# Kernel tuning notes

Measured on AMD Instinct MI355X. Metric: run time of the kernel, lower is better.

Reference implementation:

```python
import jax, jax.numpy as jnp
import numpy as np

N_HEADS = 16
WINDOW = 128
EPS = 1e-6
NEG_INF = -1e30  # effectively -inf after softmax in fp32


def setup_inputs() -> dict:
    key = jax.random.key(0)
    ks = jax.random.split(key, 5)
    B, T, D = 2, 2048, 1024
    scale = 1.0 / np.sqrt(D)
    return {
        "x": jax.random.normal(ks[0], (B, T, D), dtype=jnp.float32),
        "Wq": jax.random.normal(ks[1], (D, D), dtype=jnp.float32) * scale,
        "Wk": jax.random.normal(ks[2], (D, D), dtype=jnp.float32) * scale,
        "Wv": jax.random.normal(ks[3], (D, D), dtype=jnp.float32) * scale,
        "Wo": jax.random.normal(ks[4], (D, D), dtype=jnp.float32) * scale,
    }


def _l2norm(t):
    # torch F.normalize: t / max(||t||, eps)
    n = jnp.sqrt(jnp.sum(t * t, axis=-1, keepdims=True))
    return t / jnp.maximum(n, EPS)


def reference(x, Wq, Wk, Wv, Wo):
    B, T, D = x.shape
    H, hd = N_HEADS, D // N_HEADS
    # projections (torch Linear: x @ W.T), split heads -> [B, H, T, hd]
    def proj(W):
        return jnp.einsum('btd,ed->bte', x, W).reshape(B, T, H, hd).transpose(0, 2, 1, 3)
    q = _l2norm(proj(Wq))
    k = _l2norm(proj(Wk))
    v = proj(Wv)
    # scores [B, H, T, T] (no 1/sqrt(d) scale in the source)
    attn = jnp.einsum('bhqd,bhkd->bhqk', q, k)
    pos = jnp.arange(T)
    rel = pos[None, :] - pos[:, None]            # rel[i, j] = j - i
    mask = (rel < 0) | (rel >= WINDOW)           # allowed: 0 <= j-i < window
    base = jnp.linspace(0.0, 1.0, H, dtype=x.dtype)
    slopes = jnp.power(jnp.asarray(2.0, x.dtype), -(8.0 * base))  # [H]
    alibi = -jnp.abs(rel).astype(x.dtype)[None, :, :] * slopes[:, None, None]  # [H,T,T]
    bias = jnp.where(mask[None, :, :], jnp.asarray(NEG_INF, x.dtype), alibi)
    attn = jax.nn.softmax(attn + bias[None], axis=-1)
    out = jnp.einsum('bhqk,bhkd->bhqd', attn, v)
    out = out.transpose(0, 2, 1, 3).reshape(B, T, D)
    return jnp.einsum('btd,ed->bte', out, Wo)
```

## Files before the change

### kernel.cpp

```cpp
#include <hip/hip_runtime.h>
#include <hip/hip_bf16.h>

#define T_SEQ   2048
#define BATCH   2
#define DMODEL  1024
#define NHEADS  16
#define HDIM    64
#define WINDOW  128

typedef __attribute__((ext_vector_type(8))) short bf16x8;
typedef __attribute__((ext_vector_type(4))) float f32x4;

__device__ inline void unpack8(uint4 u, float* f) {
    unsigned int w[4] = {u.x, u.y, u.z, u.w};
#pragma unroll
    for (int i = 0; i < 4; i++) {
        f[2*i]   = __uint_as_float(w[i] << 16);
        f[2*i+1] = __uint_as_float(w[i] & 0xffff0000u);
    }
}

__device__ inline void gld_lds16(const __hip_bfloat16* g, __hip_bfloat16* l) {
    __builtin_amdgcn_global_load_lds(
        (const __attribute__((address_space(1))) unsigned int*)g,
        (__attribute__((address_space(3))) unsigned int*)l, 16, 0, 0);
}

__global__ __launch_bounds__(256) void cvt_kernel(
    const float* __restrict__ x,  const float* __restrict__ Wq,
    const float* __restrict__ Wk, const float* __restrict__ Wv,
    const float* __restrict__ Wo,
    __hip_bfloat16* __restrict__ xb, __hip_bfloat16* __restrict__ Wb)
{
    const int slot = blockIdx.y;
    const float* src;
    __hip_bfloat16* dst;
    int n;
    if (slot == 0) { src = x; dst = xb; n = 4 * 1024 * 1024; }
    else {
        src = (slot == 1) ? Wq : (slot == 2) ? Wk : (slot == 3) ? Wv : Wo;
        dst = Wb + (size_t)(slot - 1) * 1024 * 1024;
        n = 1024 * 1024;
    }
    int i = (blockIdx.x * 256 + threadIdx.x) * 8;
    if (i >= n) return;
    float4 a = *(const float4*)(src + i);
    float4 b = *(const float4*)(src + i + 4);
    __hip_bfloat16 pk[8] = {
        __float2bfloat16(a.x), __float2bfloat16(a.y),
        __float2bfloat16(a.z), __float2bfloat16(a.w),
        __float2bfloat16(b.x), __float2bfloat16(b.y),
        __float2bfloat16(b.z), __float2bfloat16(b.w)};
    *(uint4*)(dst + i) = *(uint4*)pk;
}

__global__ __launch_bounds__(256) void gemm_qkv(
    const __hip_bfloat16* __restrict__ A,
    const __hip_bfloat16* __restrict__ W0,
    const __hip_bfloat16* __restrict__ W1,
    const __hip_bfloat16* __restrict__ W2,
    __hip_bfloat16* __restrict__ C0,
    __hip_bfloat16* __restrict__ C1,
    __hip_bfloat16* __restrict__ C2,
    int M, int N, int K)
{
    const int z = blockIdx.z;
    const __hip_bfloat16* W = (z == 0) ? W0 : (z == 1 ? W1 : W2);
    __hip_bfloat16* C = (z == 0) ? C0 : (z == 1 ? C1 : C2);

    const int n0 = blockIdx.x * 128;
    const int m0 = blockIdx.y * 128;

    __shared__ __hip_bfloat16 As[128 * 32];
    __shared__ __hip_bfloat16 Bs[128 * 32];

    const int t    = threadIdx.x;
    const int lane = t & 63;
    const int wv   = t >> 6;

    const int gc   = ((lane & 3) - (lane >> 3)) & 3;
    const int srow = wv * 32 + (lane >> 2);
    const __hip_bfloat16* Ag = A + (size_t)(m0 + srow) * K + gc * 8;
    const __hip_bfloat16* Wg = W + (size_t)(n0 + srow) * K + gc * 8;
    const size_t row16 = (size_t)16 * K;
    __hip_bfloat16* AsD0 = &As[(wv * 32) * 32];
    __hip_bfloat16* AsD1 = &As[(wv * 32 + 16) * 32];
    __hip_bfloat16* BsD0 = &Bs[(wv * 32) * 32];
    __hip_bfloat16* BsD1 = &Bs[(wv * 32 + 16) * 32];

    const int wm   = (wv >> 1) * 64;
    const int wn   = (wv & 1) * 64;
    const int lrow = lane & 15;
    const int quad = lane >> 4;
    const int slot = ((quad + (lrow >> 1)) & 3) * 8;

    f32x4 acc[4][4];
#pragma unroll
    for (int i = 0; i < 4; i++)
#pragma unroll
        for (int j = 0; j < 4; j++)
            acc[i][j] = (f32x4){0.f, 0.f, 0.f, 0.f};

    for (int k0 = 0; k0 < K; k0 += 32) {
        gld_lds16(Ag + k0,         AsD0);
        gld_lds16(Ag + k0 + row16, AsD1);
        gld_lds16(Wg + k0,         BsD0);
        gld_lds16(Wg + k0 + row16, BsD1);
        __syncthreads();

        bf16x8 af[4], bfv[4];
#pragma unroll
        for (int mi = 0; mi < 4; mi++)
            af[mi] = *(const bf16x8*)&As[(wm + mi * 16 + lrow) * 32 + slot];
#pragma unroll
        for (int ni = 0; ni < 4; ni++)
            bfv[ni] = *(const bf16x8*)&Bs[(wn + ni * 16 + lrow) * 32 + slot];
#pragma unroll
        for (int mi = 0; mi < 4; mi++)
#pragma unroll
            for (int ni = 0; ni < 4; ni++)
                acc[mi][ni] = __builtin_amdgcn_mfma_f32_16x16x32_bf16(
                    af[mi], bfv[ni], acc[mi][ni], 0, 0, 0);
        __syncthreads();
    }

    if (z != 2) {
#pragma unroll
        for (int mi = 0; mi < 4; mi++) {
#pragma unroll
            for (int rr = 0; rr < 4; rr++) {
                float ss = 0.f;
#pragma unroll
                for (int ni = 0; ni < 4; ni++)
                    ss += acc[mi][ni][rr] * acc[mi][ni][rr];
                ss += __shfl_xor(ss, 1);
                ss += __shfl_xor(ss, 2);
                ss += __shfl_xor(ss, 4);
                ss += __shfl_xor(ss, 8);
                float inv = 1.0f / fmaxf(sqrtf(ss), 1e-6f);
#pragma unroll
                for (int ni = 0; ni < 4; ni++)
                    acc[mi][ni][rr] *= inv;
            }
        }
    }

#pragma unroll
    for (int mi = 0; mi < 4; mi++) {
#pragma unroll
        for (int rr = 0; rr < 4; rr++) {
            int row = m0 + wm + mi * 16 + quad * 4 + rr;
            __hip_bfloat16* Crow = C + (size_t)row * N + n0 + wn + lrow;
#pragma unroll
            for (int ni = 0; ni < 4; ni++)
                Crow[ni * 16] = __float2bfloat16(acc[mi][ni][rr]);
        }
    }
}

__global__ __launch_bounds__(256) void gemm_o(
    const __hip_bfloat16* __restrict__ A,
    const __hip_bfloat16* __restrict__ W,
    float* __restrict__ C,
    int M, int N, int K)
{
    const int n0 = blockIdx.x * 128;
    const int m0 = blockIdx.y * 64;

    __shared__ __hip_bfloat16 As[64 * 32];
    __shared__ __hip_bfloat16 Bs[128 * 32];

    const int t    = threadIdx.x;
    const int lane = t & 63;
    const int wv   = t >> 6;

    const int gc    = ((lane & 3) - (lane >> 3)) & 3;
    const int srowA = wv * 16 + (lane >> 2);
    const int srowB = wv * 32 + (lane >> 2);
    const __hip_bfloat16* Ag = A + (size_t)(m0 + srowA) * K + gc * 8;
    const __hip_bfloat16* Wg = W + (size_t)(n0 + srowB) * K + gc * 8;
    const size_t row16 = (size_t)16 * K;
    __hip_bfloat16* AsD0 = &As[(wv * 16) * 32];
    __hip_bfloat16* BsD0 = &Bs[(wv * 32) * 32];
    __hip_bfloat16* BsD1 = &Bs[(wv * 32 + 16) * 32];

    const int wm   = (wv >> 1) * 32;
    const int wn   = (wv & 1) * 64;
    const int lrow = lane & 15;
    const int quad = lane >> 4;
    const int slot = ((quad + (lrow >> 1)) & 3) * 8;

    f32x4 acc[2][4];
#pragma unroll
    for (int i = 0; i < 2; i++)
#pragma unroll
        for (int j = 0; j < 4; j++)
            acc[i][j] = (f32x4){0.f, 0.f, 0.f, 0.f};

    for (int k0 = 0; k0 < K; k0 += 32) {
        gld_lds16(Ag + k0, AsD0);
        gld_lds16(Wg + k0,         BsD0);
        gld_lds16(Wg + k0 + row16, BsD1);
        __syncthreads();

        bf16x8 af[2], bfv[4];
#pragma unroll
        for (int mi = 0; mi < 2; mi++)
            af[mi] = *(const bf16x8*)&As[(wm + mi * 16 + lrow) * 32 + slot];
#pragma unroll
        for (int ni = 0; ni < 4; ni++)
            bfv[ni] = *(const bf16x8*)&Bs[(wn + ni * 16 + lrow) * 32 + slot];
#pragma unroll
        for (int mi = 0; mi < 2; mi++)
#pragma unroll
            for (int ni = 0; ni < 4; ni++)
                acc[mi][ni] = __builtin_amdgcn_mfma_f32_16x16x32_bf16(
                    af[mi], bfv[ni], acc[mi][ni], 0, 0, 0);
        __syncthreads();
    }

#pragma unroll
    for (int mi = 0; mi < 2; mi++) {
#pragma unroll
        for (int rr = 0; rr < 4; rr++) {
            int row = m0 + wm + mi * 16 + quad * 4 + rr;
            float* Crow = C + (size_t)row * N + n0 + wn + lrow;
#pragma unroll
            for (int ni = 0; ni < 4; ni++)
                Crow[ni * 16] = acc[mi][ni][rr];
        }
    }
}

__global__ __launch_bounds__(256) void attn_kernel(
    const __hip_bfloat16* __restrict__ Q,
    const __hip_bfloat16* __restrict__ K,
    const __hip_bfloat16* __restrict__ V,
    __hip_bfloat16* __restrict__ O)
{
    const int i0 = blockIdx.x * 64;
    const int h  = blockIdx.y;
    const int b  = blockIdx.z;

    __shared__ __hip_bfloat16 Ks[192 * 72];
    __shared__ __hip_bfloat16 Vt[64 * 200];

    const size_t base = ((size_t)b * T_SEQ) * DMODEL + h * HDIM;
    const int t = threadIdx.x;

    for (int task = t; task < 192 * 8; task += 256) {
        int row = task >> 3;
        int c   = task & 7;
        int j   = min(i0 + row, T_SEQ - 1);
        *(uint4*)&Ks[row * 72 + c * 8] = *(const uint4*)(K + base + (size_t)j * DMODEL + c * 8);
    }
    for (int task = t; task < 192; task += 256) {
        int c  = task & 7;
        int r0 = (task >> 3) * 8;
        int b0 = task >> 3;
        unsigned short m[8][8];
#pragma unroll
        for (int i = 0; i < 8; i++) {
            int j = min(i0 + r0 + i, T_SEQ - 1);
            uint4 u = *(const uint4*)(V + base + (size_t)j * DMODEL + c * 8);
            unsigned short tmp[8];
            *(uint4*)tmp = u;
#pragma unroll
            for (int e = 0; e < 8; e++) m[e][i] = tmp[e];
        }
#pragma unroll
        for (int e = 0; e < 8; e++) {
            int d  = c * 8 + e;
            int sg = (b0 & ~7) | ((b0 + (d >> 3)) & 7);
            *(uint4*)&Vt[d * 200 + sg * 8] = *(uint4*)m[e];
        }
    }
    for (int task = t; task < 64; task += 256) {
        uint4 zz = {0, 0, 0, 0};
        *(uint4*)&Vt[task * 200 + 192] = zz;
    }
    __syncthreads();

    const int lane = t & 63;
    const int w    = t >> 6;
    const int col  = lane & 15;
    const int quad = lane >> 4;
    const float slope = exp2f(-8.0f * (float)h / 15.0f);

    const __hip_bfloat16* qp = Q + base + (size_t)(i0 + w * 16 + col) * DMODEL + quad * 8;
    bf16x8 qf0 = *(const bf16x8*)(qp);
    bf16x8 qf1 = *(const bf16x8*)(qp + 32);

    f32x4 sc[9];
#pragma unroll
    for (int kt = 0; kt < 9; kt++) {
        sc[kt] = (f32x4){0.f, 0.f, 0.f, 0.f};
        const __hip_bfloat16* kr = &Ks[(w * 16 + kt * 16 + col) * 72 + quad * 8];
        bf16x8 kb0 = *(const bf16x8*)(kr);
        bf16x8 kb1 = *(const bf16x8*)(kr + 32);
        sc[kt] = __builtin_amdgcn_mfma_f32_16x16x32_bf16(qf0, kb0, sc[kt], 0, 0, 0);
        sc[kt] = __builtin_amdgcn_mfma_f32_16x16x32_bf16(qf1, kb1, sc[kt], 0, 0, 0);
    }

    float mx[4] = {-3e38f, -3e38f, -3e38f, -3e38f};
#pragma unroll
    for (int kt = 0; kt < 9; kt++) {
#pragma unroll
        for (int r = 0; r < 4; r++) {
            int ql  = quad * 4 + r;
            int rel = kt * 16 + col - ql;
            int ka  = i0 + w * 16 + kt * 16 + col;
            bool valid = (rel >= 0) && (rel < WINDOW) && (ka < T_SEQ);
            float v = valid ? (sc[kt][r] - (float)rel * slope) : -1e30f;
            sc[kt][r] = v;
            mx[r] = fmaxf(mx[r], v);
        }
    }
#pragma unroll
    for (int r = 0; r < 4; r++) {
        mx[r] = fmaxf(mx[r], __shfl_xor(mx[r], 1));
        mx[r] = fmaxf(mx[r], __shfl_xor(mx[r], 2));
        mx[r] = fmaxf(mx[r], __shfl_xor(mx[r], 4));
        mx[r] = fmaxf(mx[r], __shfl_xor(mx[r], 8));
    }
    float sm[4] = {0.f, 0.f, 0.f, 0.f};
#pragma unroll
    for (int kt = 0; kt < 9; kt++) {
#pragma unroll
        for (int r = 0; r < 4; r++) {
            float e = __expf(sc[kt][r] - mx[r]);
            sc[kt][r] = e;
            sm[r] += e;
        }
    }
#pragma unroll
    for (int r = 0; r < 4; r++) {
        sm[r] += __shfl_xor(sm[r], 1);
        sm[r] += __shfl_xor(sm[r], 2);
        sm[r] += __shfl_xor(sm[r], 4);
        sm[r] += __shfl_xor(sm[r], 8);
        sm[r] = 1.0f / sm[r];
    }

    __syncthreads();
    __hip_bfloat16* Ps = Ks + w * (16 * 168);
#pragma unroll
    for (int kt = 0; kt < 9; kt++)
#pragma unroll
        for (int r = 0; r < 4; r++)
            Ps[(quad * 4 + r) * 168 + kt * 16 + col] = __float2bfloat16(sc[kt][r] * sm[r]);
#pragma unroll
    for (int i = 0; i < 4; i++)
        Ps[(lane & 15) * 168 + 144 + quad * 4 + i] = __float2bfloat16(0.f);
    __syncthreads();

    f32x4 o[4];
#pragma unroll
    for (int nd = 0; nd < 4; nd++) o[nd] = (f32x4){0.f, 0.f, 0.f, 0.f};
#pragma unroll
    for (int kc = 0; kc < 5; kc++) {
        bf16x8 pf = *(const bf16x8*)&Ps[col * 168 + kc * 32 + quad * 8];
        int bblk = w * 2 + kc * 4 + quad;
#pragma unroll
        for (int nd = 0; nd < 4; nd++) {
            int d  = nd * 16 + col;
            int sg = (bblk < 24) ? ((bblk & ~7) | ((bblk + (d >> 3)) & 7)) : 24;
            bf16x8 vf = *(const bf16x8*)&Vt[d * 200 + sg * 8];
            o[nd] = __builtin_amdgcn_mfma_f32_16x16x32_bf16(pf, vf, o[nd], 0, 0, 0);
        }
    }

#pragma unroll
    for (int r = 0; r < 4; r++) {
        __hip_bfloat16* op = O + base + (size_t)(i0 + w * 16 + quad * 4 + r) * DMODEL + col;
#pragma unroll
        for (int nd = 0; nd < 4; nd++)
            op[nd * 16] = __float2bfloat16(o[nd][r]);
    }
}

extern "C" void kernel_launch(void* const* d_in, const int* in_sizes, int n_in,
                              void* d_out, int out_size, void* d_ws, size_t ws_size,
                              hipStream_t stream)
{
    const float* x  = (const float*)d_in[0];
    const float* Wq = (const float*)d_in[1];
    const float* Wk = (const float*)d_in[2];
    const float* Wv = (const float*)d_in[3];
    const float* Wo = (const float*)d_in[4];
    float* out = (float*)d_out;

    const size_t MT = (size_t)BATCH * T_SEQ;
    __hip_bfloat16* Qw = (__hip_bfloat16*)d_ws;
    __hip_bfloat16* Kw = Qw + MT * DMODEL;
    __hip_bfloat16* Vw = Kw + MT * DMODEL;
    __hip_bfloat16* XA = Vw + MT * DMODEL;
    __hip_bfloat16* Wb = XA + MT * DMODEL;

    cvt_kernel<<<dim3(2048, 5), 256, 0, stream>>>(x, Wq, Wk, Wv, Wo, XA, Wb);

    dim3 g1(DMODEL / 128, MT / 128, 3);
    gemm_qkv<<<g1, 256, 0, stream>>>(
        XA, Wb, Wb + 1024 * 1024, Wb + 2 * 1024 * 1024,
        Qw, Kw, Vw, (int)MT, DMODEL, DMODEL);

    dim3 g2(T_SEQ / 64, NHEADS, BATCH);
    attn_kernel<<<g2, 256, 0, stream>>>(Qw, Kw, Vw, XA);

    dim3 g3(DMODEL / 128, MT / 64, 1);
    gemm_o<<<g3, 256, 0, stream>>>(
        XA, Wb + 3 * 1024 * 1024, out, (int)MT, DMODEL, DMODEL);
}
```

Before: 155.7 us.

## Remap GEMM tiles per XCD and load attention K via direct-to-LDS swizzle

Both GEMMs now derive tile coordinates from a linearized block id so that consecutive blocks dispatched to the same XCD cover a compact M×N region. This is meant to improve L2 reuse of A and W rows within each XCD's cache. The attention kernel loads its K tile with global_load_lds into an unpadded, XOR-style swizzled LDS layout instead of staging through registers into a padded layout. The MFMA reads use the matching swizzle. This cuts register traffic and LDS footprint, but the new mappings assume specific grid dimensions.

```diff
diff --git a/kernel.cpp b/kernel.cpp
--- a/kernel.cpp
+++ b/kernel.cpp
@@ -64,12 +64,19 @@
     __hip_bfloat16* __restrict__ C2,
     int M, int N, int K)
 {
-    const int z = blockIdx.z;
+    const int lid   = blockIdx.x + 8 * blockIdx.y + 256 * blockIdx.z;
+    const int xcd   = lid & 7;
+    const int s     = lid >> 3;
+    const int m_loc = s & 7;
+    const int rest  = s >> 3;
+    const int n_loc = rest & 3;
+    const int z     = rest >> 2;
+
     const __hip_bfloat16* W = (z == 0) ? W0 : (z == 1 ? W1 : W2);
     __hip_bfloat16* C = (z == 0) ? C0 : (z == 1 ? C1 : C2);
 
-    const int n0 = blockIdx.x * 128;
-    const int m0 = blockIdx.y * 128;
+    const int m0 = ((xcd & 3) * 8 + m_loc) * 128;
+    const int n0 = ((xcd >> 2) * 4 + n_loc) * 128;
 
     __shared__ __hip_bfloat16 As[128 * 32];
     __shared__ __hip_bfloat16 Bs[128 * 32];
@@ -164,8 +171,14 @@
     float* __restrict__ C,
     int M, int N, int K)
 {
-    const int n0 = blockIdx.x * 128;
-    const int m0 = blockIdx.y * 64;
+    const int lid   = blockIdx.x + 8 * blockIdx.y;
+    const int xcd   = lid & 7;
+    const int s     = lid >> 3;
+    const int m_loc = s & 15;
+    const int n_loc = s >> 4;
+
+    const int m0 = ((xcd & 3) * 16 + m_loc) * 64;
+    const int n0 = ((xcd >> 2) * 4 + n_loc) * 128;
 
     __shared__ __hip_bfloat16 As[64 * 32];
     __shared__ __hip_bfloat16 Bs[128 * 32];
@@ -242,17 +255,24 @@
     const int h  = blockIdx.y;
     const int b  = blockIdx.z;
 
-    __shared__ __hip_bfloat16 Ks[192 * 72];
+    __shared__ __hip_bfloat16 Ks[192 * 64];
     __shared__ __hip_bfloat16 Vt[64 * 200];
 
     const size_t base = ((size_t)b * T_SEQ) * DMODEL + h * HDIM;
-    const int t = threadIdx.x;
-
-    for (int task = t; task < 192 * 8; task += 256) {
-        int row = task >> 3;
-        int c   = task & 7;
-        int j   = min(i0 + row, T_SEQ - 1);
-        *(uint4*)&Ks[row * 72 + c * 8] = *(const uint4*)(K + base + (size_t)j * DMODEL + c * 8);
+    const int t    = threadIdx.x;
+    const int lane = t & 63;
+    const int w    = t >> 6;
+
+    {
+        const int drow = lane >> 3, sl = lane & 7;
+#pragma unroll
+        for (int inst = 0; inst < 6; inst++) {
+            int r0 = w * 48 + inst * 8;
+            int r  = r0 + drow;
+            int gcx = (sl - r) & 7;
+            int j  = min(i0 + r, T_SEQ - 1);
+            gld_lds16(K + base + (size_t)j * DMODEL + gcx * 8, &Ks[r0 * 64]);
+        }
     }
     for (int task = t; task < 192; task += 256) {
         int c  = task & 7;
@@ -281,8 +301,6 @@
     }
     __syncthreads();
 
-    const int lane = t & 63;
-    const int w    = t >> 6;
     const int col  = lane & 15;
     const int quad = lane >> 4;
     const float slope = exp2f(-8.0f * (float)h / 15.0f);
@@ -295,9 +313,9 @@
 #pragma unroll
     for (int kt = 0; kt < 9; kt++) {
         sc[kt] = (f32x4){0.f, 0.f, 0.f, 0.f};
-        const __hip_bfloat16* kr = &Ks[(w * 16 + kt * 16 + col) * 72 + quad * 8];
-        bf16x8 kb0 = *(const bf16x8*)(kr);
-        bf16x8 kb1 = *(const bf16x8*)(kr + 32);
+        int r = w * 16 + kt * 16 + col;
+        bf16x8 kb0 = *(const bf16x8*)&Ks[r * 64 + ((quad     + r) & 7) * 8];
+        bf16x8 kb1 = *(const bf16x8*)&Ks[r * 64 + ((quad + 4 + r) & 7) * 8];
         sc[kt] = __builtin_amdgcn_mfma_f32_16x16x32_bf16(qf0, kb0, sc[kt], 0, 0, 0);
         sc[kt] = __builtin_amdgcn_mfma_f32_16x16x32_bf16(qf1, kb1, sc[kt], 0, 0, 0);
     }
```

After: 153.8 us. About the same (-1.3%).
